# Performance work log

Measured on AMD Instinct MI355X. Metric: run time of the kernel, lower is better.

The kernel has to match this reference:

```python
import jax, jax.numpy as jnp
import numpy as np

DEGREE = 3
FEATURES = 512
N_BSPLINES = 64
BATCH = 2048
WINDOW = DEGREE + 2  # unfold window size: degree + 2
N_KNOTS = N_BSPLINES + DEGREE + 1


def setup_inputs() -> dict:
    key = jax.random.key(0)
    kx, kw = jax.random.split(key)
    x = jax.random.uniform(kx, (BATCH, FEATURES), dtype=jnp.float32)  # in [0,1] = interval
    # reset_parameter(): linspace over interval broadcast to all features
    knots = jnp.broadcast_to(
        jnp.linspace(0.0, 1.0, N_KNOTS, dtype=jnp.float32), (FEATURES, N_KNOTS)
    )
    # weights are zero-init in the module; use small random values for a meaningful baseline
    weights = jax.random.normal(kw, (FEATURES, N_BSPLINES), dtype=jnp.float32) * 0.1
    return {"x": x, "knots": knots, "weights": weights}


def reference(x, knots, weights):
    # knots.unfold(-1, degree+2, 1) -> (F, N, W) sliding windows
    idx = jnp.arange(N_BSPLINES)[:, None] + jnp.arange(WINDOW)[None, :]  # (N, W)
    kwin = knots[:, idx]  # (F, N, W)
    # relu^degree of (x - knot) differences: (B, F, N, W)
    relu = jnp.maximum(x[..., None, None] - kwin, 0.0) ** DEGREE
    # pairwise knot differences + eye: dif[i, j] = kwin[j] - kwin[i] + delta_ij
    knot_dif = kwin[..., None, :] - kwin[..., :, None] + jnp.eye(WINDOW, dtype=knots.dtype)  # (F, N, W, W)
    coef = 1.0 / jnp.prod(knot_dif, axis=-1)  # (F, N, W) divided-difference coefficients
    spline = jnp.sum(relu * coef, axis=-1)  # vecdot over window -> (B, F, N)
    return jnp.sum(spline * weights, axis=-1)  # vecdot over splines -> (B, F)
```

## Files before the change

### kernel.cpp

```cpp
#include <hip/hip_runtime.h>

#pragma clang fp contract(off)

#define FEATURES   512
#define N_BSPLINES 64
#define N_KNOTS    68
#define WINDOW     5
#define BATCH      2048

__device__ __forceinline__ float cube_f32(float r) {
    float s = r * r;
    return s * r;
}

__global__ __launch_bounds__(N_BSPLINES * WINDOW) void bspline_prep(
    const float* __restrict__ knots, float* __restrict__ coef)
{
    const int f = blockIdx.x;
    const int t = threadIdx.x;
    const int i = t / WINDOW, j = t % WINDOW;
    const float* kf = knots + f * N_KNOTS;
    const float kj = kf[i + j];
    float prod = 1.0f;
    #pragma unroll
    for (int b = 0; b < WINDOW; ++b) {
        float df = (b == j) ? 1.0f : (kf[i + b] - kj);
        prod = prod * df;
    }
    coef[f * (N_BSPLINES * WINDOW) + t] = 1.0f / prod;
}

__global__ __launch_bounds__(256, 8) void bspline_eval(
    const float* __restrict__ x, const float* __restrict__ knots,
    const float* __restrict__ coef, const float* __restrict__ weights,
    float* __restrict__ out)
{
    const int f  = blockIdx.x & (FEATURES - 1);
    const int bc = blockIdx.x >> 9;
    const int b  = bc * 256 + threadIdx.x;

    const float* __restrict__ kf = knots   + f * N_KNOTS;
    const float* __restrict__ cf = coef    + f * (N_BSPLINES * WINDOW);
    const float* __restrict__ wf = weights + f * N_BSPLINES;

    const float xv = x[b * FEATURES + f];
    float acc = 0.0f;
    float r0 = cube_f32(fmaxf(xv - kf[0], 0.0f));
    float r1 = cube_f32(fmaxf(xv - kf[1], 0.0f));
    float r2 = cube_f32(fmaxf(xv - kf[2], 0.0f));
    float r3 = cube_f32(fmaxf(xv - kf[3], 0.0f));
    float r4 = cube_f32(fmaxf(xv - kf[4], 0.0f));

    #pragma unroll
    for (int i = 0; i < N_BSPLINES; ++i) {
        float m0 = r0 * cf[i * WINDOW + 0];
        float m1 = r1 * cf[i * WINDOW + 1];
        float m2 = r2 * cf[i * WINDOW + 2];
        float m3 = r3 * cf[i * WINDOW + 3];
        float m4 = r4 * cf[i * WINDOW + 4];
        float t04  = m0 + m4;
        float t042 = t04 + m2;
        float t13  = m1 + m3;
        float sp   = t042 + t13;
        acc = acc + sp * wf[i];
        r0 = r1; r1 = r2; r2 = r3; r3 = r4;
        if (i < N_BSPLINES - 1)
            r4 = cube_f32(fmaxf(xv - kf[i + 5], 0.0f));
    }

    out[b * FEATURES + f] = acc;
}

extern "C" void kernel_launch(void* const* d_in, const int* in_sizes, int n_in,
                              void* d_out, int out_size, void* d_ws, size_t ws_size,
                              hipStream_t stream) {
    const float* x       = (const float*)d_in[0];
    const float* knots   = (const float*)d_in[1];
    const float* weights = (const float*)d_in[2];
    float*       out     = (float*)d_out;
    float*       coef    = (float*)d_ws;

    bspline_prep<<<FEATURES, N_BSPLINES * WINDOW, 0, stream>>>(knots, coef);

    const int blocks = FEATURES * (BATCH / 256);
    bspline_eval<<<blocks, 256, 0, stream>>>(x, knots, coef, weights, out);
}
```

Baseline: 84.29 us.

## Fuse coefficient prep into eval kernel with LDS-staged coefs and two rows per thread

Drops the separate prep kernel. Each block now computes the divided-difference coefficients for its feature into shared memory, packed with the weights into 8-float rows so each spline step reads one float4 and one float2. Each thread evaluates two batch rows, which halves the block count and spreads the per-block prep cost across more work. The trade-off is that coefficients are recomputed in every block rather than once per feature, plus an added barrier.

```diff
diff --git a/kernel.cpp b/kernel.cpp
--- a/kernel.cpp
+++ b/kernel.cpp
@@ -7,68 +7,97 @@
 #define N_KNOTS    68
 #define WINDOW     5
 #define BATCH      2048
+#define ROWSTRIDE  8
 
 __device__ __forceinline__ float cube_f32(float r) {
     float s = r * r;
     return s * r;
 }
 
-__global__ __launch_bounds__(N_BSPLINES * WINDOW) void bspline_prep(
-    const float* __restrict__ knots, float* __restrict__ coef)
+__global__ __launch_bounds__(256, 8) void bspline_fused(
+    const float* __restrict__ x, const float* __restrict__ knots,
+    const float* __restrict__ weights, float* __restrict__ out)
 {
-    const int f = blockIdx.x;
-    const int t = threadIdx.x;
-    const int i = t / WINDOW, j = t % WINDOW;
-    const float* kf = knots + f * N_KNOTS;
-    const float kj = kf[i + j];
-    float prod = 1.0f;
-    #pragma unroll
-    for (int b = 0; b < WINDOW; ++b) {
-        float df = (b == j) ? 1.0f : (kf[i + b] - kj);
-        prod = prod * df;
-    }
-    coef[f * (N_BSPLINES * WINDOW) + t] = 1.0f / prod;
-}
+    __shared__ __align__(16) float cw[N_BSPLINES * ROWSTRIDE];
 
-__global__ __launch_bounds__(256, 8) void bspline_eval(
-    const float* __restrict__ x, const float* __restrict__ knots,
-    const float* __restrict__ coef, const float* __restrict__ weights,
-    float* __restrict__ out)
-{
-    const int f  = blockIdx.x & (FEATURES - 1);
-    const int bc = blockIdx.x >> 9;
-    const int b  = bc * 256 + threadIdx.x;
+    const int f   = blockIdx.x & (FEATURES - 1);
+    const int bc  = blockIdx.x >> 9;
+    const int tid = threadIdx.x;
 
     const float* __restrict__ kf = knots   + f * N_KNOTS;
-    const float* __restrict__ cf = coef    + f * (N_BSPLINES * WINDOW);
     const float* __restrict__ wf = weights + f * N_BSPLINES;
 
-    const float xv = x[b * FEATURES + f];
-    float acc = 0.0f;
-    float r0 = cube_f32(fmaxf(xv - kf[0], 0.0f));
-    float r1 = cube_f32(fmaxf(xv - kf[1], 0.0f));
-    float r2 = cube_f32(fmaxf(xv - kf[2], 0.0f));
-    float r3 = cube_f32(fmaxf(xv - kf[3], 0.0f));
-    float r4 = cube_f32(fmaxf(xv - kf[4], 0.0f));
+    {
+        auto coef_at = [&](int t) {
+            const int i = t / WINDOW, j = t % WINDOW;
+            const float kj = kf[i + j];
+            float prod = 1.0f;
+            #pragma unroll
+            for (int b = 0; b < WINDOW; ++b) {
+                float df = (b == j) ? 1.0f : (kf[i + b] - kj);
+                prod = prod * df;
+            }
+            cw[i * ROWSTRIDE + (t % WINDOW)] = 1.0f / prod;
+        };
+        coef_at(tid);
+        if (tid < N_BSPLINES * WINDOW - 256)
+            coef_at(tid + 256);
+        if (tid < N_BSPLINES)
+            cw[tid * ROWSTRIDE + WINDOW] = wf[tid];
+    }
+    __syncthreads();
 
+    const int b0 = bc * 512 + tid;
+    const float xv0 = x[b0 * FEATURES + f];
+    const float xv1 = x[(b0 + 256) * FEATURES + f];
+
+    float r0[WINDOW], r1[WINDOW];
+    #pragma unroll
+    for (int t = 0; t < WINDOW; ++t) {
+        r0[t] = cube_f32(fmaxf(xv0 - kf[t], 0.0f));
+        r1[t] = cube_f32(fmaxf(xv1 - kf[t], 0.0f));
+    }
+
+    float acc0 = 0.0f, acc1 = 0.0f;
     #pragma unroll
     for (int i = 0; i < N_BSPLINES; ++i) {
-        float m0 = r0 * cf[i * WINDOW + 0];
-        float m1 = r1 * cf[i * WINDOW + 1];
-        float m2 = r2 * cf[i * WINDOW + 2];
-        float m3 = r3 * cf[i * WINDOW + 3];
-        float m4 = r4 * cf[i * WINDOW + 4];
-        float t04  = m0 + m4;
-        float t042 = t04 + m2;
-        float t13  = m1 + m3;
-        float sp   = t042 + t13;
-        acc = acc + sp * wf[i];
-        r0 = r1; r1 = r2; r2 = r3; r3 = r4;
-        if (i < N_BSPLINES - 1)
-            r4 = cube_f32(fmaxf(xv - kf[i + 5], 0.0f));
+        const float4 c03 = *reinterpret_cast<const float4*>(&cw[i * ROWSTRIDE]);
+        const float2 c4w = *reinterpret_cast<const float2*>(&cw[i * ROWSTRIDE + 4]);
+
+        {
+            float m0 = r0[0] * c03.x;
+            float m1 = r0[1] * c03.y;
+            float m2 = r0[2] * c03.z;
+            float m3 = r0[3] * c03.w;
+            float m4 = r0[4] * c4w.x;
+            float t04  = m0 + m4;
+            float t042 = t04 + m2;
+            float t13  = m1 + m3;
+            float sp   = t042 + t13;
+            acc0 = acc0 + sp * c4w.y;
+        }
+        {
+            float m0 = r1[0] * c03.x;
+            float m1 = r1[1] * c03.y;
+            float m2 = r1[2] * c03.z;
+            float m3 = r1[3] * c03.w;
+            float m4 = r1[4] * c4w.x;
+            float t04  = m0 + m4;
+            float t042 = t04 + m2;
+            float t13  = m1 + m3;
+            float sp   = t042 + t13;
+            acc1 = acc1 + sp * c4w.y;
+        }
+        #pragma unroll
+        for (int t = 0; t < WINDOW - 1; ++t) { r0[t] = r0[t + 1]; r1[t] = r1[t + 1]; }
+        if (i < N_BSPLINES - 1) {
+            r0[WINDOW - 1] = cube_f32(fmaxf(xv0 - kf[i + WINDOW], 0.0f));
+            r1[WINDOW - 1] = cube_f32(fmaxf(xv1 - kf[i + WINDOW], 0.0f));
+        }
     }
 
-    out[b * FEATURES + f] = acc;
+    out[b0 * FEATURES + f] = acc0;
+    out[(b0 + 256) * FEATURES + f] = acc1;
 }
 
 extern "C" void kernel_launch(void* const* d_in, const int* in_sizes, int n_in,
@@ -78,10 +107,8 @@
     const float* knots   = (const float*)d_in[1];
     const float* weights = (const float*)d_in[2];
     float*       out     = (float*)d_out;
-    float*       coef    = (float*)d_ws;
+    (void)d_ws; (void)ws_size;
 
-    bspline_prep<<<FEATURES, N_BSPLINES * WINDOW, 0, stream>>>(knots, coef);
-
-    const int blocks = FEATURES * (BATCH / 256);
-    bspline_eval<<<blocks, 256, 0, stream>>>(x, knots, coef, weights, out);
+    const int blocks = FEATURES * (BATCH / 512);
+    bspline_fused<<<blocks, 256, 0, stream>>>(x, knots, weights, out);
 }
```

Measured after the change: 128.1 us. 1.52x slower.

## Pack coef/weight/knot table, stage in LDS, compute four rows per thread

Applied to the files above, without the earlier changes.

The prep kernel now writes one packed per-feature table (5 coefficients, weight, next knot, padding) in 8-float rows. The eval kernel handles 16 features by 64 rows per block and copies the table into padded shared memory with float4 loads. Each thread then evaluates four batch rows, so every coefficient load is reused four times. Global accesses to x and out are now coalesced across the feature dimension. The cost is more registers, hence launch bounds lowered to 4 waves, and the shared-memory footprint limits occupancy.

```diff
diff --git a/kernel.cpp b/kernel.cpp
--- a/kernel.cpp
+++ b/kernel.cpp
@@ -7,19 +7,27 @@
 #define N_KNOTS    68
 #define WINDOW     5
 #define BATCH      2048
+#define ROWSTRIDE  8
+#define F_PER_F    512
+#define FPB        16
+#define RPB        64
+#define TBL_STRIDE 516
 
 __device__ __forceinline__ float cube_f32(float r) {
     float s = r * r;
     return s * r;
 }
 
-__global__ __launch_bounds__(N_BSPLINES * WINDOW) void bspline_prep(
-    const float* __restrict__ knots, float* __restrict__ coef)
+__global__ __launch_bounds__(320) void bspline_prep(
+    const float* __restrict__ knots, const float* __restrict__ weights,
+    float* __restrict__ tbl)
 {
     const int f = blockIdx.x;
     const int t = threadIdx.x;
-    const int i = t / WINDOW, j = t % WINDOW;
-    const float* kf = knots + f * N_KNOTS;
+    const float* __restrict__ kf = knots + f * N_KNOTS;
+    float* __restrict__ tf = tbl + f * F_PER_F;
+
+    const int i = t / WINDOW, j = t - i * WINDOW;
     const float kj = kf[i + j];
     float prod = 1.0f;
     #pragma unroll
@@ -27,48 +35,145 @@
         float df = (b == j) ? 1.0f : (kf[i + b] - kj);
         prod = prod * df;
     }
-    coef[f * (N_BSPLINES * WINDOW) + t] = 1.0f / prod;
+    tf[i * ROWSTRIDE + j] = 1.0f / prod;
+
+    if (t < N_BSPLINES) {
+        tf[t * ROWSTRIDE + 5] = weights[f * N_BSPLINES + t];
+        tf[t * ROWSTRIDE + 6] = (t < N_BSPLINES - 1) ? kf[t + WINDOW] : 0.0f;
+        tf[t * ROWSTRIDE + 7] = 0.0f;
+    }
 }
 
-__global__ __launch_bounds__(256, 8) void bspline_eval(
+__global__ __launch_bounds__(256, 4) void bspline_eval(
     const float* __restrict__ x, const float* __restrict__ knots,
-    const float* __restrict__ coef, const float* __restrict__ weights,
-    float* __restrict__ out)
+    const float* __restrict__ tbl, float* __restrict__ out)
 {
-    const int f  = blockIdx.x & (FEATURES - 1);
-    const int bc = blockIdx.x >> 9;
-    const int b  = bc * 256 + threadIdx.x;
+    __shared__ __align__(16) float lt[FPB * TBL_STRIDE];
 
-    const float* __restrict__ kf = knots   + f * N_KNOTS;
-    const float* __restrict__ cf = coef    + f * (N_BSPLINES * WINDOW);
-    const float* __restrict__ wf = weights + f * N_BSPLINES;
+    const int fgrp  = blockIdx.x & 31;
+    const int bgrp  = blockIdx.x >> 5;
+    const int f0    = fgrp * FPB;
+    const int rbase = bgrp * RPB;
+    const int t     = threadIdx.x;
+    const int fl    = t & (FPB - 1);
+    const int rl    = t >> 4;
 
-    const float xv = x[b * FEATURES + f];
-    float acc = 0.0f;
-    float r0 = cube_f32(fmaxf(xv - kf[0], 0.0f));
-    float r1 = cube_f32(fmaxf(xv - kf[1], 0.0f));
-    float r2 = cube_f32(fmaxf(xv - kf[2], 0.0f));
-    float r3 = cube_f32(fmaxf(xv - kf[3], 0.0f));
-    float r4 = cube_f32(fmaxf(xv - kf[4], 0.0f));
+    {
+        const float4* __restrict__ src = reinterpret_cast<const float4*>(tbl);
+        float4* dst = reinterpret_cast<float4*>(lt);
+        #pragma unroll
+        for (int c = 0; c < 8; ++c) {
+            const int idx = c * 256 + t;
+            const int f   = idx >> 7;
+            const int pos = idx & 127;
+            dst[f * 129 + pos] = src[(f0 + f) * 128 + pos];
+        }
+    }
+    __syncthreads();
+
+    const int ff = f0 + fl;
+    const float* __restrict__ kfp = knots + ff * N_KNOTS;
+    const float kf0 = kfp[0], kf1 = kfp[1], kf2 = kfp[2],
+                kf3 = kfp[3], kf4 = kfp[4];
+
+    const float xvA = x[(rbase + rl     ) * FEATURES + ff];
+    const float xvB = x[(rbase + rl + 16) * FEATURES + ff];
+    const float xvC = x[(rbase + rl + 32) * FEATURES + ff];
+    const float xvD = x[(rbase + rl + 48) * FEATURES + ff];
+
+    float wa0 = cube_f32(fmaxf(xvA - kf0, 0.0f));
+    float wa1 = cube_f32(fmaxf(xvA - kf1, 0.0f));
+    float wa2 = cube_f32(fmaxf(xvA - kf2, 0.0f));
+    float wa3 = cube_f32(fmaxf(xvA - kf3, 0.0f));
+    float wa4 = cube_f32(fmaxf(xvA - kf4, 0.0f));
+    float wb0 = cube_f32(fmaxf(xvB - kf0, 0.0f));
+    float wb1 = cube_f32(fmaxf(xvB - kf1, 0.0f));
+    float wb2 = cube_f32(fmaxf(xvB - kf2, 0.0f));
+    float wb3 = cube_f32(fmaxf(xvB - kf3, 0.0f));
+    float wb4 = cube_f32(fmaxf(xvB - kf4, 0.0f));
+    float wc0 = cube_f32(fmaxf(xvC - kf0, 0.0f));
+    float wc1 = cube_f32(fmaxf(xvC - kf1, 0.0f));
+    float wc2 = cube_f32(fmaxf(xvC - kf2, 0.0f));
+    float wc3 = cube_f32(fmaxf(xvC - kf3, 0.0f));
+    float wc4 = cube_f32(fmaxf(xvC - kf4, 0.0f));
+    float wd0 = cube_f32(fmaxf(xvD - kf0, 0.0f));
+    float wd1 = cube_f32(fmaxf(xvD - kf1, 0.0f));
+    float wd2 = cube_f32(fmaxf(xvD - kf2, 0.0f));
+    float wd3 = cube_f32(fmaxf(xvD - kf3, 0.0f));
+    float wd4 = cube_f32(fmaxf(xvD - kf4, 0.0f));
+
+    float accA = 0.0f, accB = 0.0f, accC = 0.0f, accD = 0.0f;
+    const float4* __restrict__ ltf =
+        reinterpret_cast<const float4*>(lt) + fl * 129;
 
     #pragma unroll
     for (int i = 0; i < N_BSPLINES; ++i) {
-        float m0 = r0 * cf[i * WINDOW + 0];
-        float m1 = r1 * cf[i * WINDOW + 1];
-        float m2 = r2 * cf[i * WINDOW + 2];
-        float m3 = r3 * cf[i * WINDOW + 3];
-        float m4 = r4 * cf[i * WINDOW + 4];
-        float t04  = m0 + m4;
-        float t042 = t04 + m2;
-        float t13  = m1 + m3;
-        float sp   = t042 + t13;
-        acc = acc + sp * wf[i];
-        r0 = r1; r1 = r2; r2 = r3; r3 = r4;
-        if (i < N_BSPLINES - 1)
-            r4 = cube_f32(fmaxf(xv - kf[i + 5], 0.0f));
+        const float4 cA = ltf[i * 2];
+        const float4 cB = ltf[i * 2 + 1];
+
+        {
+            float m0 = wa0 * cA.x;
+            float m1 = wa1 * cA.y;
+            float m2 = wa2 * cA.z;
+            float m3 = wa3 * cA.w;
+            float m4 = wa4 * cB.x;
+            float t04  = m0 + m4;
+            float t042 = t04 + m2;
+            float t13  = m1 + m3;
+            float sp   = t042 + t13;
+            accA = accA + sp * cB.y;
+        }
+        {
+            float m0 = wb0 * cA.x;
+            float m1 = wb1 * cA.y;
+            float m2 = wb2 * cA.z;
+            float m3 = wb3 * cA.w;
+            float m4 = wb4 * cB.x;
+            float t04  = m0 + m4;
+            float t042 = t04 + m2;
+            float t13  = m1 + m3;
+            float sp   = t042 + t13;
+            accB = accB + sp * cB.y;
+        }
+        {
+            float m0 = wc0 * cA.x;
+            float m1 = wc1 * cA.y;
+            float m2 = wc2 * cA.z;
+            float m3 = wc3 * cA.w;
+            float m4 = wc4 * cB.x;
+            float t04  = m0 + m4;
+            float t042 = t04 + m2;
+            float t13  = m1 + m3;
+            float sp   = t042 + t13;
+            accC = accC + sp * cB.y;
+        }
+        {
+            float m0 = wd0 * cA.x;
+            float m1 = wd1 * cA.y;
+            float m2 = wd2 * cA.z;
+            float m3 = wd3 * cA.w;
+            float m4 = wd4 * cB.x;
+            float t04  = m0 + m4;
+            float t042 = t04 + m2;
+            float t13  = m1 + m3;
+            float sp   = t042 + t13;
+            accD = accD + sp * cB.y;
+        }
+
+        wa0 = wa1; wa1 = wa2; wa2 = wa3; wa3 = wa4;
+        wb0 = wb1; wb1 = wb2; wb2 = wb3; wb3 = wb4;
+        wc0 = wc1; wc1 = wc2; wc2 = wc3; wc3 = wc4;
+        wd0 = wd1; wd1 = wd2; wd2 = wd3; wd3 = wd4;
+        wa4 = cube_f32(fmaxf(xvA - cB.z, 0.0f));
+        wb4 = cube_f32(fmaxf(xvB - cB.z, 0.0f));
+        wc4 = cube_f32(fmaxf(xvC - cB.z, 0.0f));
+        wd4 = cube_f32(fmaxf(xvD - cB.z, 0.0f));
     }
 
-    out[b * FEATURES + f] = acc;
+    out[(rbase + rl     ) * FEATURES + ff] = accA;
+    out[(rbase + rl + 16) * FEATURES + ff] = accB;
+    out[(rbase + rl + 32) * FEATURES + ff] = accC;
+    out[(rbase + rl + 48) * FEATURES + ff] = accD;
 }
 
 extern "C" void kernel_launch(void* const* d_in, const int* in_sizes, int n_in,
@@ -78,10 +183,10 @@
     const float* knots   = (const float*)d_in[1];
     const float* weights = (const float*)d_in[2];
     float*       out     = (float*)d_out;
-    float*       coef    = (float*)d_ws;
+    float*       tbl     = (float*)d_ws;
 
-    bspline_prep<<<FEATURES, N_BSPLINES * WINDOW, 0, stream>>>(knots, coef);
+    bspline_prep<<<FEATURES, 320, 0, stream>>>(knots, weights, tbl);
 
-    const int blocks = FEATURES * (BATCH / 256);
-    bspline_eval<<<blocks, 256, 0, stream>>>(x, knots, coef, weights, out);
+    const int blocks = (FEATURES / FPB) * (BATCH / RPB);
+    bspline_eval<<<blocks, 256, 0, stream>>>(x, knots, tbl, out);
 }
```

After: 81.33 us. -3.5%, faster.
